# Optimization experiments

Measured on AMD Instinct MI355X. Metric: run time of the kernel, lower is better.

## Reference

```python
import jax, jax.numpy as jnp
import numpy as np

B, S, D, H = 2, 2048, 1024, 16
HD = D // H  # head_dim = 64


def setup_inputs() -> dict:
    key = jax.random.key(0)
    ks = jax.random.split(key, 11)
    init = 1.0 / np.sqrt(D)
    inp = {
        "query": jax.random.normal(ks[0], (B, S, D), jnp.float32),
        "key": jax.random.normal(ks[1], (B, S, D), jnp.float32),
        "value": jax.random.normal(ks[2], (B, S, D), jnp.float32),
        "Wq": jax.random.uniform(ks[3], (D, D), jnp.float32, -init, init),
        "bq": jax.random.uniform(ks[4], (D,), jnp.float32, -init, init),
        "Wk": jax.random.uniform(ks[5], (D, D), jnp.float32, -init, init),
        "bk": jax.random.uniform(ks[6], (D,), jnp.float32, -init, init),
        "Wv": jax.random.uniform(ks[7], (D, D), jnp.float32, -init, init),
        "bv": jax.random.uniform(ks[8], (D,), jnp.float32, -init, init),
        "Wo": jax.random.uniform(ks[9], (D, D), jnp.float32, -init, init),
        "bo": jax.random.uniform(ks[10], (D,), jnp.float32, -init, init),
    }
    return inp


def reference(query, key, value, Wq, bq, Wk, bk, Wv, bv, Wo, bo):
    # Linear projections (torch Linear: x @ W.T + b)
    q = query @ Wq.T + bq  # [B,S,D]
    k = key @ Wk.T + bk
    v = value @ Wv.T + bv
    # split heads -> [B,H,S,HD]
    q = q.reshape(B, S, H, HD).transpose(0, 2, 1, 3)
    k = k.reshape(B, S, H, HD).transpose(0, 2, 1, 3)
    v = v.reshape(B, S, H, HD).transpose(0, 2, 1, 3)
    # NOTE: original code divides by scale = head_dim**-0.5, i.e. multiplies
    # scores by sqrt(head_dim). Reproduced faithfully.
    scale = HD ** (-0.5)
    scores = jnp.einsum("bhqd,bhkd->bhqk", q, k) / scale  # [B,H,S,S]
    attn = jax.nn.softmax(scores, axis=-1)
    x = jnp.einsum("bhqk,bhkd->bhqd", attn, v)  # [B,H,S,HD]
    x = x.transpose(0, 2, 1, 3).reshape(B, S, D)
    return x @ Wo.T + bo
```

## Files before the change

kernel.cpp:

```cpp
#include <hip/hip_runtime.h>
#include <stdint.h>
#include <stddef.h>

#define SCALE_LOG2E 11.541560327111707f
#define E8 4194304
#define M1 1048576
#define NROW 65536

typedef __attribute__((ext_vector_type(8))) _Float16 f16x8;
typedef __attribute__((ext_vector_type(4))) _Float16 f16x4;
typedef __attribute__((ext_vector_type(4))) float f32x4;

#if __has_builtin(__builtin_amdgcn_exp2f)
#define EXP2F(x) __builtin_amdgcn_exp2f(x)
#else
#define EXP2F(x) exp2f(x)
#endif

__device__ __forceinline__ f32x4 mfma_f16(f16x8 a, f16x8 b, f32x4 c) {
  return __builtin_amdgcn_mfma_f32_16x16x32_f16(a, b, c, 0, 0, 0);
}

__device__ __forceinline__ f32x4 mfma16_f16(f16x4 a, f16x4 b, f32x4 c) {
  return __builtin_amdgcn_mfma_f32_16x16x16f16(a, b, c, 0, 0, 0);
}

__device__ __forceinline__ void async16(const void* g, void* lds) {
  __builtin_amdgcn_global_load_lds(
      (const __attribute__((address_space(1))) unsigned int*)g,
      (__attribute__((address_space(3))) unsigned int*)lds, 16, 0, 0);
}

__global__ void prep_all(const float* __restrict__ q, const float* __restrict__ k,
                         const float* __restrict__ v,
                         const float* __restrict__ wq, const float* __restrict__ wk,
                         const float* __restrict__ wv, const float* __restrict__ wo,
                         _Float16* __restrict__ Xf, _Float16* __restrict__ Wf) {
  const int gid = blockIdx.x;
  const float* src;
  _Float16* dst;
  int i;
  if (gid < 6144) {
    const int z = gid >> 11;
    src = (z == 0) ? q : (z == 1) ? k : v;
    dst = Xf + (size_t)z * E8;
    i = (gid & 2047) * 512 + threadIdx.x;
  } else {
    const int g2 = gid - 6144;
    const int z = g2 >> 9;
    src = (z == 0) ? wq : (z == 1) ? wk : (z == 2) ? wv : wo;
    dst = Wf + (size_t)z * M1;
    i = (g2 & 511) * 512 + threadIdx.x;
  }
#pragma unroll
  for (int off = 0; off < 512; off += 256) {
    float4 x = ((const float4*)src)[i + off];
    f16x4 h = {(_Float16)x.x, (_Float16)x.y, (_Float16)x.z, (_Float16)x.w};
    ((f16x4*)dst)[i + off] = h;
  }
}

__global__ __launch_bounds__(256, 3) void gemm_qkv(
    const _Float16* __restrict__ Xf,
    const _Float16* __restrict__ Wf,
    const float* __restrict__ bq, const float* __restrict__ bk,
    const float* __restrict__ bv,
    _Float16* __restrict__ Of)
{
  __shared__ _Float16 SMEM[16384];
  _Float16* LA = SMEM;
  _Float16* LB = SMEM + 8192;
  const int z = blockIdx.z;
  const int tid = threadIdx.x;
  const int lane = tid & 63;
  const int wv = tid >> 6;
  const int wm = wv >> 1, wn = wv & 1;
  const int rl = lane & 15, qd = lane >> 4;
  const int m0 = blockIdx.x * 128, n0 = blockIdx.y * 128;

  const _Float16* A0 = Xf + (size_t)z * E8;
  const _Float16* W0 = Wf + (size_t)z * M1;
  const float* bias = (z == 0) ? bq : (z == 1) ? bk : bv;

  f32x4 acc[4][4];
#pragma unroll
  for (int i = 0; i < 4; i++)
#pragma unroll
    for (int j = 0; j < 4; j++) acc[i][j] = f32x4{0.f, 0.f, 0.f, 0.f};

  const int srow = wv * 32 + (lane >> 2);
  const int scol = (lane & 3) * 8;

  auto stage = [&](int k0, int buf) {
    const _Float16* ga = A0 + (size_t)(m0 + srow) * 1024 + k0 + scol;
    async16(ga, &LA[buf * 4096 + wv * 1024]);
    async16(ga + 16 * 1024, &LA[buf * 4096 + wv * 1024 + 512]);
    const _Float16* gb = W0 + (size_t)(n0 + srow) * 1024 + k0 + scol;
    async16(gb, &LB[buf * 4096 + wv * 1024]);
    async16(gb + 16 * 1024, &LB[buf * 4096 + wv * 1024 + 512]);
  };

  stage(0, 0);
  for (int t = 0; t < 32; t++) {
    const int buf = t & 1;
    __syncthreads();
    if (t + 1 < 32) stage((t + 1) * 32, buf ^ 1);
    f16x8 af[4], bfr[4];
#pragma unroll
    for (int i = 0; i < 4; i++) af[i] = *(const f16x8*)&LA[buf * 4096 + (wm * 64 + i * 16 + rl) * 32 + qd * 8];
#pragma unroll
    for (int j = 0; j < 4; j++) bfr[j] = *(const f16x8*)&LB[buf * 4096 + (wn * 64 + j * 16 + rl) * 32 + qd * 8];
#pragma unroll
    for (int i = 0; i < 4; i++)
#pragma unroll
      for (int j = 0; j < 4; j++) acc[i][j] = mfma_f16(af[i], bfr[j], acc[i][j]);
  }

  if (z == 2) {
#pragma unroll
    for (int j = 0; j < 4; j++) {
      const int nn = n0 + wn * 64 + j * 16 + rl;
      const float bj = bias[nn];
      const int hh = nn >> 6, e = nn & 63;
#pragma unroll
      for (int i = 0; i < 4; i++) {
        const int mm = m0 + wm * 64 + i * 16 + qd * 4;
        const int b = mm >> 11, s = mm & 2047;
        f16x4 pk = {(_Float16)(acc[i][j][0] + bj), (_Float16)(acc[i][j][1] + bj),
                    (_Float16)(acc[i][j][2] + bj), (_Float16)(acc[i][j][3] + bj)};
        *(f16x4*)(Of + 2 * (size_t)E8 + (((size_t)((b * 16 + hh) * 64 + e)) << 11) + s) = pk;
      }
    }
  } else {
    const float scl = (z == 0) ? SCALE_LOG2E : 1.0f;
    _Float16* base = Of + (size_t)z * E8;
    __syncthreads();
#pragma unroll
    for (int j = 0; j < 4; j++) {
      const int nl = wn * 64 + j * 16 + rl;
      const float bj = bias[n0 + nl];
#pragma unroll
      for (int i = 0; i < 4; i++) {
        const int ml = wm * 64 + i * 16 + qd * 4;
        const int np = nl ^ (qd << 4);
#pragma unroll
        for (int r = 0; r < 4; r++)
          SMEM[(ml + r) * 128 + np] = (_Float16)((acc[i][j][r] + bj) * scl);
      }
    }
    __syncthreads();
#pragma unroll
    for (int it2 = 0; it2 < 8; it2++) {
      const int m = (it2 * 256 + tid) >> 4;
      const int col8 = (tid & 15) * 8;
      const int np = col8 ^ (((m >> 2) & 3) << 4);
      f16x8 vrow = *(const f16x8*)&SMEM[m * 128 + np];
      const int sg = m0 + m;
      const int b = sg >> 11, s = sg & 2047;
      const int nn = n0 + col8;
      const int hh = nn >> 6, e = nn & 63;
      *(f16x8*)(base + (((size_t)((b * 16 + hh) * 2048 + s)) << 6) + e) = vrow;
    }
  }
}

__global__ __launch_bounds__(256, 4) void attn_kernel(
    const _Float16* __restrict__ Qb,
    const _Float16* __restrict__ Kb,
    const _Float16* __restrict__ Vt,
    float* __restrict__ Op,
    float2* __restrict__ ML)
{
  __shared__ _Float16 Ks[2][4096];
  __shared__ _Float16 Vs[2][4096];
  const int tid = threadIdx.x;
  const int lane = tid & 63;
  const int wv = tid >> 6;
  const int rl = lane & 15, qd = lane >> 4;
  const int bh = blockIdx.x;
  const int half = blockIdx.z;
  const int kvb = half * 1024;
  const int q0 = blockIdx.y * 128 + wv * 32;

  f16x8 qf[2][2];
#pragma unroll
  for (int mt = 0; mt < 2; mt++)
#pragma unroll
    for (int kk = 0; kk < 2; kk++)
      qf[mt][kk] = *(const f16x8*)(Qb + ((size_t)bh * 2048 + q0 + mt * 16 + rl) * 64 +
                                   kk * 32 + qd * 8);

  float m_[2] = {-1e30f, -1e30f}, l_[2] = {0.f, 0.f};
  f32x4 o[2][4];
#pragma unroll
  for (int mt = 0; mt < 2; mt++)
#pragma unroll
    for (int jt = 0; jt < 4; jt++) o[mt][jt] = f32x4{0.f, 0.f, 0.f, 0.f};

  auto stage = [&](int kv, int buf) {
#pragma unroll
    for (int it = 0; it < 2; it++) {
      const int cI = it * 256 + tid;
      const int row = cI >> 3;
      const int c = (cI & 7) ^ (row & 7);
      const int dst = (it * 256 + wv * 64) * 8;
      async16(Kb + ((size_t)bh * 2048 + kv + row) * 64 + c * 8, &Ks[buf][dst]);
      async16(Vt + ((size_t)bh * 64 + row) * 2048 + kv + c * 8, &Vs[buf][dst]);
    }
  };

  stage(kvb, 0);

  for (int t = 0; t < 16; t++) {
    const int buf = t & 1;
    __syncthreads();
    if (t + 1 < 16) stage(kvb + (t + 1) * 64, buf ^ 1);

    f32x4 sc[2][4];
#pragma unroll
    for (int mt = 0; mt < 2; mt++)
#pragma unroll
      for (int nt = 0; nt < 4; nt++) sc[mt][nt] = f32x4{0.f, 0.f, 0.f, 0.f};
    __builtin_amdgcn_s_setprio(1);
#pragma unroll
    for (int nt = 0; nt < 4; nt++) {
      const int ro = (nt * 16 + rl) * 64;
#pragma unroll
      for (int kk = 0; kk < 2; kk++) {
        const int cc = (((kk * 4 + qd) ^ (rl & 7)) << 3);
        f16x8 kh = *(const f16x8*)&Ks[buf][ro + cc];
#pragma unroll
        for (int mt = 0; mt < 2; mt++)
          sc[mt][nt] = mfma_f16(kh, qf[mt][kk], sc[mt][nt]);
      }
    }
    __builtin_amdgcn_s_setprio(0);

    f16x4 pf[2][4];
#pragma unroll
    for (int mt = 0; mt < 2; mt++) {
      float a0 = fmaxf(fmaxf(sc[mt][0][0], sc[mt][0][1]), fmaxf(sc[mt][0][2], sc[mt][0][3]));
      float a1 = fmaxf(fmaxf(sc[mt][1][0], sc[mt][1][1]), fmaxf(sc[mt][1][2], sc[mt][1][3]));
      float a2 = fmaxf(fmaxf(sc[mt][2][0], sc[mt][2][1]), fmaxf(sc[mt][2][2], sc[mt][2][3]));
      float a3 = fmaxf(fmaxf(sc[mt][3][0], sc[mt][3][1]), fmaxf(sc[mt][3][2], sc[mt][3][3]));
      float mloc = fmaxf(fmaxf(a0, a1), fmaxf(a2, a3));
      float mx = fmaxf(mloc, __shfl_xor(mloc, 16));
      mx = fmaxf(mx, __shfl_xor(mx, 32));
      const float mold = m_[mt];
      float mnew = mold;
      if (__any(mx > mold + 8.f)) {
        mnew = fmaxf(mold, mx);
        const float al = EXP2F(mold - mnew);
        l_[mt] *= al;
#pragma unroll
        for (int jt = 0; jt < 4; jt++)
#pragma unroll
          for (int r = 0; r < 4; r++) o[mt][jt][r] *= al;
        m_[mt] = mnew;
      }
      float sm = 0.f;
#pragma unroll
      for (int nt = 0; nt < 4; nt++) {
        const float p0 = EXP2F(sc[mt][nt][0] - mnew);
        const float p1 = EXP2F(sc[mt][nt][1] - mnew);
        const float p2 = EXP2F(sc[mt][nt][2] - mnew);
        const float p3 = EXP2F(sc[mt][nt][3] - mnew);
        sm += (p0 + p1) + (p2 + p3);
        pf[mt][nt] = f16x4{(_Float16)p0, (_Float16)p1, (_Float16)p2, (_Float16)p3};
      }
      l_[mt] += sm;
    }

    __builtin_amdgcn_s_setprio(1);
#pragma unroll
    for (int nt = 0; nt < 4; nt++) {
      const int cb = nt * 2 + (qd >> 1);
#pragma unroll
      for (int jt = 0; jt < 4; jt++) {
        const int row = jt * 16 + rl;
        f16x4 vvv = *(const f16x4*)&Vs[buf][row * 64 + ((cb ^ (rl & 7)) << 3) + (qd & 1) * 4];
        o[0][jt] = mfma16_f16(vvv, pf[0][nt], o[0][jt]);
        o[1][jt] = mfma16_f16(vvv, pf[1][nt], o[1][jt]);
      }
    }
    __builtin_amdgcn_s_setprio(0);
  }

#pragma unroll
  for (int mt = 0; mt < 2; mt++) {
    float lt = l_[mt] + __shfl_xor(l_[mt], 16);
    lt += __shfl_xor(lt, 32);
    const size_t row = (size_t)bh * 2048 + q0 + mt * 16 + rl;
    float* op = Op + ((size_t)half * NROW + row) * 64;
#pragma unroll
    for (int jt = 0; jt < 4; jt++)
      *(f32x4*)(op + jt * 16 + qd * 4) = o[mt][jt];
    if (qd == 0) ML[(size_t)half * NROW + row] = make_float2(m_[mt], lt);
  }
}

__global__ void merge_kernel(const float* __restrict__ Op,
                             const float2* __restrict__ ML,
                             _Float16* __restrict__ Xo) {
  const int t = threadIdx.x;
  const int row = blockIdx.x * 16 + (t >> 4);
  const int d0 = (t & 15) * 4;
  const float2 ml1 = ML[row];
  const float2 ml2 = ML[NROW + row];
  const float m = fmaxf(ml1.x, ml2.x);
  const float w1 = EXP2F(ml1.x - m), w2 = EXP2F(ml2.x - m);
  const float inv = 1.0f / (ml1.y * w1 + ml2.y * w2);
  const float4 o1 = *(const float4*)(Op + (size_t)row * 64 + d0);
  const float4 o2 = *(const float4*)(Op + (size_t)NROW * 64 + (size_t)row * 64 + d0);
  const int bh = row >> 11, q = row & 2047;
  const int b = bh >> 4, hh = bh & 15;
  f16x4 pk = {(_Float16)((o1.x * w1 + o2.x * w2) * inv),
              (_Float16)((o1.y * w1 + o2.y * w2) * inv),
              (_Float16)((o1.z * w1 + o2.z * w2) * inv),
              (_Float16)((o1.w * w1 + o2.w * w2) * inv)};
  *(f16x4*)(Xo + ((size_t)(b * 2048 + q)) * 1024 + hh * 64 + d0) = pk;
}

__global__ __launch_bounds__(256, 2) void gemm_out(
    const _Float16* __restrict__ A0,
    const _Float16* __restrict__ W0,
    const float* __restrict__ bias,
    float* __restrict__ out)
{
  __shared__ _Float16 LA[2][2048];
  __shared__ _Float16 LB[2][4096];
  const int tid = threadIdx.x;
  const int lane = tid & 63;
  const int wv = tid >> 6;
  const int wm = wv >> 1, wn = wv & 1;
  const int rl = lane & 15, qd = lane >> 4;
  const int m0 = blockIdx.x * 64, n0 = blockIdx.y * 128;

  f32x4 acc[2][4];
#pragma unroll
  for (int i = 0; i < 2; i++)
#pragma unroll
    for (int j = 0; j < 4; j++) acc[i][j] = f32x4{0.f, 0.f, 0.f, 0.f};

  auto stage = [&](int k0, int buf) {
    {
      const int row = tid >> 2, c = tid & 3;
      async16(A0 + (size_t)(m0 + row) * 1024 + k0 + c * 8, &LA[buf][wv * 512]);
    }
#pragma unroll
    for (int it = 0; it < 2; it++) {
      const int cI = it * 256 + tid;
      const int row = cI >> 2, c = cI & 3;
      async16(W0 + (size_t)(n0 + row) * 1024 + k0 + c * 8,
              &LB[buf][it * 2048 + wv * 512]);
    }
  };

  stage(0, 0);
  for (int t = 0; t < 32; t++) {
    const int buf = t & 1;
    __syncthreads();
    if (t + 1 < 32) stage((t + 1) * 32, buf ^ 1);
    f16x8 af[2], bfr[4];
#pragma unroll
    for (int i = 0; i < 2; i++) af[i] = *(const f16x8*)&LA[buf][(wm * 32 + i * 16 + rl) * 32 + qd * 8];
#pragma unroll
    for (int j = 0; j < 4; j++) bfr[j] = *(const f16x8*)&LB[buf][(wn * 64 + j * 16 + rl) * 32 + qd * 8];
#pragma unroll
    for (int i = 0; i < 2; i++)
#pragma unroll
      for (int j = 0; j < 4; j++) acc[i][j] = mfma_f16(af[i], bfr[j], acc[i][j]);
  }

#pragma unroll
  for (int j = 0; j < 4; j++) {
    const int nn = n0 + wn * 64 + j * 16 + rl;
    const float bj = bias[nn];
#pragma unroll
    for (int i = 0; i < 2; i++) {
      const int mm = m0 + wm * 32 + i * 16 + qd * 4;
#pragma unroll
      for (int r = 0; r < 4; r++)
        out[(size_t)(mm + r) * 1024 + nn] = acc[i][j][r] + bj;
    }
  }
}

extern "C" void kernel_launch(void* const* d_in, const int* in_sizes, int n_in,
                              void* d_out, int out_size, void* d_ws, size_t ws_size,
                              hipStream_t stream) {
  const float* query = (const float*)d_in[0];
  const float* key   = (const float*)d_in[1];
  const float* value = (const float*)d_in[2];
  const float* Wq = (const float*)d_in[3];
  const float* bq = (const float*)d_in[4];
  const float* Wk = (const float*)d_in[5];
  const float* bk = (const float*)d_in[6];
  const float* Wv = (const float*)d_in[7];
  const float* bv = (const float*)d_in[8];
  const float* Wo = (const float*)d_in[9];
  const float* bo = (const float*)d_in[10];

  _Float16* ws = (_Float16*)d_ws;
  _Float16* Xf = ws;
  _Float16* Wf = ws + 3 * (size_t)E8;
  _Float16* Qh = Wf + 4 * (size_t)M1;
  _Float16* Kh = Qh + (size_t)E8;
  _Float16* Vt = Kh + (size_t)E8;
  _Float16* Xa = Vt + (size_t)E8;
  float*    Op = (float*)(Xa + (size_t)E8);
  float2*   ML = (float2*)(Op + 2 * (size_t)NROW * 64);

  prep_all<<<8192, 256, 0, stream>>>(query, key, value, Wq, Wk, Wv, Wo, Xf, Wf);
  gemm_qkv<<<dim3(32, 8, 3), 256, 0, stream>>>(Xf, Wf, bq, bk, bv, Qh);
  attn_kernel<<<dim3(32, 16, 2), 256, 0, stream>>>(Qh, Kh, Vt, Op, ML);
  merge_kernel<<<4096, 256, 0, stream>>>(Op, ML, Xa);
  gemm_out<<<dim3(64, 8), 256, 0, stream>>>(Xa, Wf + 3 * (size_t)M1, bo, (float*)d_out);
}
```

Measured before the change: 240.9 us.

## Fuse fp32-to-fp16 activation conversion into QKV GEMM A-tile loading

```diff
diff --git a/kernel.cpp b/kernel.cpp
--- a/kernel.cpp
+++ b/kernel.cpp
@@ -31,29 +31,21 @@
       (__attribute__((address_space(3))) unsigned int*)lds, 16, 0, 0);
 }
 
-__global__ void prep_all(const float* __restrict__ q, const float* __restrict__ k,
-                         const float* __restrict__ v,
-                         const float* __restrict__ wq, const float* __restrict__ wk,
-                         const float* __restrict__ wv, const float* __restrict__ wo,
-                         _Float16* __restrict__ Xf, _Float16* __restrict__ Wf) {
+__device__ __forceinline__ f16x8 cvt8(float4 a, float4 b) {
+  return f16x8{(_Float16)a.x, (_Float16)a.y, (_Float16)a.z, (_Float16)a.w,
+               (_Float16)b.x, (_Float16)b.y, (_Float16)b.z, (_Float16)b.w};
+}
+
+__global__ void prep_w(const float* __restrict__ wq, const float* __restrict__ wk,
+                       const float* __restrict__ wv, const float* __restrict__ wo,
+                       _Float16* __restrict__ Wf) {
   const int gid = blockIdx.x;
-  const float* src;
-  _Float16* dst;
-  int i;
-  if (gid < 6144) {
-    const int z = gid >> 11;
-    src = (z == 0) ? q : (z == 1) ? k : v;
-    dst = Xf + (size_t)z * E8;
-    i = (gid & 2047) * 512 + threadIdx.x;
-  } else {
-    const int g2 = gid - 6144;
-    const int z = g2 >> 9;
-    src = (z == 0) ? wq : (z == 1) ? wk : (z == 2) ? wv : wo;
-    dst = Wf + (size_t)z * M1;
-    i = (g2 & 511) * 512 + threadIdx.x;
-  }
-#pragma unroll
-  for (int off = 0; off < 512; off += 256) {
+  const int z = gid >> 8;
+  const float* src = (z == 0) ? wq : (z == 1) ? wk : (z == 2) ? wv : wo;
+  _Float16* dst = Wf + (size_t)z * M1;
+  const int i = (gid & 255) * 1024 + threadIdx.x;
+#pragma unroll
+  for (int off = 0; off < 1024; off += 256) {
     float4 x = ((const float4*)src)[i + off];
     f16x4 h = {(_Float16)x.x, (_Float16)x.y, (_Float16)x.z, (_Float16)x.w};
     ((f16x4*)dst)[i + off] = h;
@@ -61,7 +53,8 @@
 }
 
 __global__ __launch_bounds__(256, 3) void gemm_qkv(
-    const _Float16* __restrict__ Xf,
+    const float* __restrict__ q32, const float* __restrict__ k32,
+    const float* __restrict__ v32,
     const _Float16* __restrict__ Wf,
     const float* __restrict__ bq, const float* __restrict__ bk,
     const float* __restrict__ bv,
@@ -78,7 +71,7 @@
   const int rl = lane & 15, qd = lane >> 4;
   const int m0 = blockIdx.x * 128, n0 = blockIdx.y * 128;
 
-  const _Float16* A0 = Xf + (size_t)z * E8;
+  const float* A32 = (z == 0) ? q32 : (z == 1) ? k32 : v32;
   const _Float16* W0 = Wf + (size_t)z * M1;
   const float* bias = (z == 0) ? bq : (z == 1) ? bk : bv;
 
@@ -91,20 +84,34 @@
   const int srow = wv * 32 + (lane >> 2);
   const int scol = (lane & 3) * 8;
 
-  auto stage = [&](int k0, int buf) {
-    const _Float16* ga = A0 + (size_t)(m0 + srow) * 1024 + k0 + scol;
-    async16(ga, &LA[buf * 4096 + wv * 1024]);
-    async16(ga + 16 * 1024, &LA[buf * 4096 + wv * 1024 + 512]);
+  auto stageB = [&](int k0, int buf) {
     const _Float16* gb = W0 + (size_t)(n0 + srow) * 1024 + k0 + scol;
     async16(gb, &LB[buf * 4096 + wv * 1024]);
     async16(gb + 16 * 1024, &LB[buf * 4096 + wv * 1024 + 512]);
   };
-
-  stage(0, 0);
+  auto loadA = [&](int k0, float4* ar) {
+    const float* ga = A32 + (size_t)(m0 + srow) * 1024 + k0 + scol;
+    ar[0] = *(const float4*)(ga);
+    ar[1] = *(const float4*)(ga + 4);
+    ar[2] = *(const float4*)(ga + 16 * 1024);
+    ar[3] = *(const float4*)(ga + 16 * 1024 + 4);
+  };
+  auto writeA = [&](int buf, const float4* ar) {
+    *(f16x8*)&LA[buf * 4096 + wv * 1024 + lane * 8] = cvt8(ar[0], ar[1]);
+    *(f16x8*)&LA[buf * 4096 + wv * 1024 + 512 + lane * 8] = cvt8(ar[2], ar[3]);
+  };
+
+  float4 ar[4];
+  loadA(0, ar);
+  stageB(0, 0);
+  writeA(0, ar);
   for (int t = 0; t < 32; t++) {
     const int buf = t & 1;
     __syncthreads();
-    if (t + 1 < 32) stage((t + 1) * 32, buf ^ 1);
+    if (t + 1 < 32) {
+      loadA((t + 1) * 32, ar);
+      stageB((t + 1) * 32, buf ^ 1);
+    }
     f16x8 af[4], bfr[4];
 #pragma unroll
     for (int i = 0; i < 4; i++) af[i] = *(const f16x8*)&LA[buf * 4096 + (wm * 64 + i * 16 + rl) * 32 + qd * 8];
@@ -114,6 +121,7 @@
     for (int i = 0; i < 4; i++)
 #pragma unroll
       for (int j = 0; j < 4; j++) acc[i][j] = mfma_f16(af[i], bfr[j], acc[i][j]);
+    if (t + 1 < 32) writeA(buf ^ 1, ar);
   }
 
   if (z == 2) {
@@ -402,7 +410,6 @@
   const float* bo = (const float*)d_in[10];
 
   _Float16* ws = (_Float16*)d_ws;
-  _Float16* Xf = ws;
   _Float16* Wf = ws + 3 * (size_t)E8;
   _Float16* Qh = Wf + 4 * (size_t)M1;
   _Float16* Kh = Qh + (size_t)E8;
@@ -411,8 +418,8 @@
   float*    Op = (float*)(Xa + (size_t)E8);
   float2*   ML = (float2*)(Op + 2 * (size_t)NROW * 64);
 
-  prep_all<<<8192, 256, 0, stream>>>(query, key, value, Wq, Wk, Wv, Wo, Xf, Wf);
-  gemm_qkv<<<dim3(32, 8, 3), 256, 0, stream>>>(Xf, Wf, bq, bk, bv, Qh);
+  prep_w<<<1024, 256, 0, stream>>>(Wq, Wk, Wv, Wo, Wf);
+  gemm_qkv<<<dim3(32, 8, 3), 256, 0, stream>>>(query, key, value, Wf, bq, bk, bv, Qh);
   attn_kernel<<<dim3(32, 16, 2), 256, 0, stream>>>(Qh, Kh, Vt, Op, ML);
   merge_kernel<<<4096, 256, 0, stream>>>(Op, ML, Xa);
   gemm_out<<<dim3(64, 8), 256, 0, stream>>>(Xa, Wf + 3 * (size_t)M1, bo, (float*)d_out);
```

Measured after the change: 248.6 us. +3.2%, slower.

## Fuse split-KV merge into output projection GEMM A-tile loading

Applied to the files above, without the earlier changes.

```diff
diff --git a/kernel.cpp b/kernel.cpp
--- a/kernel.cpp
+++ b/kernel.cpp
@@ -299,30 +299,9 @@
   }
 }
 
-__global__ void merge_kernel(const float* __restrict__ Op,
-                             const float2* __restrict__ ML,
-                             _Float16* __restrict__ Xo) {
-  const int t = threadIdx.x;
-  const int row = blockIdx.x * 16 + (t >> 4);
-  const int d0 = (t & 15) * 4;
-  const float2 ml1 = ML[row];
-  const float2 ml2 = ML[NROW + row];
-  const float m = fmaxf(ml1.x, ml2.x);
-  const float w1 = EXP2F(ml1.x - m), w2 = EXP2F(ml2.x - m);
-  const float inv = 1.0f / (ml1.y * w1 + ml2.y * w2);
-  const float4 o1 = *(const float4*)(Op + (size_t)row * 64 + d0);
-  const float4 o2 = *(const float4*)(Op + (size_t)NROW * 64 + (size_t)row * 64 + d0);
-  const int bh = row >> 11, q = row & 2047;
-  const int b = bh >> 4, hh = bh & 15;
-  f16x4 pk = {(_Float16)((o1.x * w1 + o2.x * w2) * inv),
-              (_Float16)((o1.y * w1 + o2.y * w2) * inv),
-              (_Float16)((o1.z * w1 + o2.z * w2) * inv),
-              (_Float16)((o1.w * w1 + o2.w * w2) * inv)};
-  *(f16x4*)(Xo + ((size_t)(b * 2048 + q)) * 1024 + hh * 64 + d0) = pk;
-}
-
 __global__ __launch_bounds__(256, 2) void gemm_out(
-    const _Float16* __restrict__ A0,
+    const float* __restrict__ Op,
+    const float2* __restrict__ ML,
     const _Float16* __restrict__ W0,
     const float* __restrict__ bias,
     float* __restrict__ out)
@@ -342,11 +321,11 @@
 #pragma unroll
     for (int j = 0; j < 4; j++) acc[i][j] = f32x4{0.f, 0.f, 0.f, 0.f};
 
-  auto stage = [&](int k0, int buf) {
-    {
-      const int row = tid >> 2, c = tid & 3;
-      async16(A0 + (size_t)(m0 + row) * 1024 + k0 + c * 8, &LA[buf][wv * 512]);
-    }
+  const int arow = tid >> 2, ac = tid & 3;
+  const int am = m0 + arow;
+  const size_t prow_b = (size_t)((am >> 11) * 16) * 2048 + (am & 2047);
+
+  auto stageB = [&](int k0, int buf) {
 #pragma unroll
     for (int it = 0; it < 2; it++) {
       const int cI = it * 256 + tid;
@@ -355,12 +334,44 @@
               &LB[buf][it * 2048 + wv * 512]);
     }
   };
-
-  stage(0, 0);
+  auto loadA = [&](int k0, f32x4* a4, float2& ml1, float2& ml2) {
+    const int hh = k0 >> 6;
+    const size_t prow = prow_b + (size_t)hh * 2048;
+    const int d0 = (k0 & 63) + ac * 8;
+    const float* p1 = Op + prow * 64 + d0;
+    const float* p2 = Op + (size_t)NROW * 64 + prow * 64 + d0;
+    a4[0] = *(const f32x4*)p1;
+    a4[1] = *(const f32x4*)(p1 + 4);
+    a4[2] = *(const f32x4*)p2;
+    a4[3] = *(const f32x4*)(p2 + 4);
+    ml1 = ML[prow];
+    ml2 = ML[NROW + prow];
+  };
+  auto writeA = [&](int buf, const f32x4* a4, float2 ml1, float2 ml2) {
+    const float mm = fmaxf(ml1.x, ml2.x);
+    const float w1 = EXP2F(ml1.x - mm), w2 = EXP2F(ml2.x - mm);
+    const float inv = 1.0f / (ml1.y * w1 + ml2.y * w2);
+    f16x8 hv;
+#pragma unroll
+    for (int j = 0; j < 4; j++) {
+      hv[j]     = (_Float16)((a4[0][j] * w1 + a4[2][j] * w2) * inv);
+      hv[j + 4] = (_Float16)((a4[1][j] * w1 + a4[3][j] * w2) * inv);
+    }
+    *(f16x8*)&LA[buf][tid * 8] = hv;
+  };
+
+  f32x4 a4[4];
+  float2 ml1, ml2;
+  loadA(0, a4, ml1, ml2);
+  stageB(0, 0);
+  writeA(0, a4, ml1, ml2);
   for (int t = 0; t < 32; t++) {
     const int buf = t & 1;
     __syncthreads();
-    if (t + 1 < 32) stage((t + 1) * 32, buf ^ 1);
+    if (t + 1 < 32) {
+      loadA((t + 1) * 32, a4, ml1, ml2);
+      stageB((t + 1) * 32, buf ^ 1);
+    }
     f16x8 af[2], bfr[4];
 #pragma unroll
     for (int i = 0; i < 2; i++) af[i] = *(const f16x8*)&LA[buf][(wm * 32 + i * 16 + rl) * 32 + qd * 8];
@@ -370,6 +381,7 @@
     for (int i = 0; i < 2; i++)
 #pragma unroll
       for (int j = 0; j < 4; j++) acc[i][j] = mfma_f16(af[i], bfr[j], acc[i][j]);
+    if (t + 1 < 32) writeA(buf ^ 1, a4, ml1, ml2);
   }
 
 #pragma unroll
@@ -414,6 +426,5 @@
   prep_all<<<8192, 256, 0, stream>>>(query, key, value, Wq, Wk, Wv, Wo, Xf, Wf);
   gemm_qkv<<<dim3(32, 8, 3), 256, 0, stream>>>(Xf, Wf, bq, bk, bv, Qh);
   attn_kernel<<<dim3(32, 16, 2), 256, 0, stream>>>(Qh, Kh, Vt, Op, ML);
-  merge_kernel<<<4096, 256, 0, stream>>>(Op, ML, Xa);
-  gemm_out<<<dim3(64, 8), 256, 0, stream>>>(Xa, Wf + 3 * (size_t)M1, bo, (float*)d_out);
-}
+  gemm_out<<<dim3(64, 8), 256, 0, stream>>>(Op, ML, Wf + 3 * (size_t)M1, bo, (float*)d_out);
+}
```

New measurement: 249.5 us. +3.5%, slower.

## Drop split-KV attention and merge kernel; process full KV per block

Applied to the files above, without the earlier changes.

```diff
diff --git a/kernel.cpp b/kernel.cpp
--- a/kernel.cpp
+++ b/kernel.cpp
@@ -5,7 +5,6 @@
 #define SCALE_LOG2E 11.541560327111707f
 #define E8 4194304
 #define M1 1048576
-#define NROW 65536
 
 typedef __attribute__((ext_vector_type(8))) _Float16 f16x8;
 typedef __attribute__((ext_vector_type(4))) _Float16 f16x4;
@@ -168,8 +167,7 @@
     const _Float16* __restrict__ Qb,
     const _Float16* __restrict__ Kb,
     const _Float16* __restrict__ Vt,
-    float* __restrict__ Op,
-    float2* __restrict__ ML)
+    _Float16* __restrict__ Xo)
 {
   __shared__ _Float16 Ks[2][4096];
   __shared__ _Float16 Vs[2][4096];
@@ -178,24 +176,17 @@
   const int wv = tid >> 6;
   const int rl = lane & 15, qd = lane >> 4;
   const int bh = blockIdx.x;
-  const int half = blockIdx.z;
-  const int kvb = half * 1024;
-  const int q0 = blockIdx.y * 128 + wv * 32;
-
-  f16x8 qf[2][2];
-#pragma unroll
-  for (int mt = 0; mt < 2; mt++)
-#pragma unroll
-    for (int kk = 0; kk < 2; kk++)
-      qf[mt][kk] = *(const f16x8*)(Qb + ((size_t)bh * 2048 + q0 + mt * 16 + rl) * 64 +
-                                   kk * 32 + qd * 8);
-
-  float m_[2] = {-1e30f, -1e30f}, l_[2] = {0.f, 0.f};
-  f32x4 o[2][4];
-#pragma unroll
-  for (int mt = 0; mt < 2; mt++)
-#pragma unroll
-    for (int jt = 0; jt < 4; jt++) o[mt][jt] = f32x4{0.f, 0.f, 0.f, 0.f};
+  const int q0 = blockIdx.y * 64 + wv * 16;
+
+  f16x8 qf[2];
+#pragma unroll
+  for (int kk = 0; kk < 2; kk++)
+    qf[kk] = *(const f16x8*)(Qb + ((size_t)bh * 2048 + q0 + rl) * 64 + kk * 32 + qd * 8);
+
+  float m_ = -1e30f, l_ = 0.f;
+  f32x4 o[4];
+#pragma unroll
+  for (int jt = 0; jt < 4; jt++) o[jt] = f32x4{0.f, 0.f, 0.f, 0.f};
 
   auto stage = [&](int kv, int buf) {
 #pragma unroll
@@ -209,18 +200,16 @@
     }
   };
 
-  stage(kvb, 0);
-
-  for (int t = 0; t < 16; t++) {
+  stage(0, 0);
+
+  for (int t = 0; t < 32; t++) {
     const int buf = t & 1;
     __syncthreads();
-    if (t + 1 < 16) stage(kvb + (t + 1) * 64, buf ^ 1);
-
-    f32x4 sc[2][4];
-#pragma unroll
-    for (int mt = 0; mt < 2; mt++)
-#pragma unroll
-      for (int nt = 0; nt < 4; nt++) sc[mt][nt] = f32x4{0.f, 0.f, 0.f, 0.f};
+    if (t + 1 < 32) stage((t + 1) * 64, buf ^ 1);
+
+    f32x4 sc[4];
+#pragma unroll
+    for (int nt = 0; nt < 4; nt++) sc[nt] = f32x4{0.f, 0.f, 0.f, 0.f};
     __builtin_amdgcn_s_setprio(1);
 #pragma unroll
     for (int nt = 0; nt < 4; nt++) {
@@ -229,46 +218,43 @@
       for (int kk = 0; kk < 2; kk++) {
         const int cc = (((kk * 4 + qd) ^ (rl & 7)) << 3);
         f16x8 kh = *(const f16x8*)&Ks[buf][ro + cc];
-#pragma unroll
-        for (int mt = 0; mt < 2; mt++)
-          sc[mt][nt] = mfma_f16(kh, qf[mt][kk], sc[mt][nt]);
+        sc[nt] = mfma_f16(kh, qf[kk], sc[nt]);
       }
     }
     __builtin_amdgcn_s_setprio(0);
 
-    f16x4 pf[2][4];
-#pragma unroll
-    for (int mt = 0; mt < 2; mt++) {
-      float a0 = fmaxf(fmaxf(sc[mt][0][0], sc[mt][0][1]), fmaxf(sc[mt][0][2], sc[mt][0][3]));
-      float a1 = fmaxf(fmaxf(sc[mt][1][0], sc[mt][1][1]), fmaxf(sc[mt][1][2], sc[mt][1][3]));
-      float a2 = fmaxf(fmaxf(sc[mt][2][0], sc[mt][2][1]), fmaxf(sc[mt][2][2], sc[mt][2][3]));
-      float a3 = fmaxf(fmaxf(sc[mt][3][0], sc[mt][3][1]), fmaxf(sc[mt][3][2], sc[mt][3][3]));
+    f16x4 pf[4];
+    {
+      float a0 = fmaxf(fmaxf(sc[0][0], sc[0][1]), fmaxf(sc[0][2], sc[0][3]));
+      float a1 = fmaxf(fmaxf(sc[1][0], sc[1][1]), fmaxf(sc[1][2], sc[1][3]));
+      float a2 = fmaxf(fmaxf(sc[2][0], sc[2][1]), fmaxf(sc[2][2], sc[2][3]));
+      float a3 = fmaxf(fmaxf(sc[3][0], sc[3][1]), fmaxf(sc[3][2], sc[3][3]));
       float mloc = fmaxf(fmaxf(a0, a1), fmaxf(a2, a3));
       float mx = fmaxf(mloc, __shfl_xor(mloc, 16));
       mx = fmaxf(mx, __shfl_xor(mx, 32));
-      const float mold = m_[mt];
+      const float mold = m_;
       float mnew = mold;
       if (__any(mx > mold + 8.f)) {
         mnew = fmaxf(mold, mx);
         const float al = EXP2F(mold - mnew);
-        l_[mt] *= al;
+        l_ *= al;
 #pragma unroll
         for (int jt = 0; jt < 4; jt++)
 #pragma unroll
-          for (int r = 0; r < 4; r++) o[mt][jt][r] *= al;
-        m_[mt] = mnew;
+          for (int r = 0; r < 4; r++) o[jt][r] *= al;
+        m_ = mnew;
       }
       float sm = 0.f;
 #pragma unroll
       for (int nt = 0; nt < 4; nt++) {
-        const float p0 = EXP2F(sc[mt][nt][0] - mnew);
-        const float p1 = EXP2F(sc[mt][nt][1] - mnew);
-        const float p2 = EXP2F(sc[mt][nt][2] - mnew);
-        const float p3 = EXP2F(sc[mt][nt][3] - mnew);
+        const float p0 = EXP2F(sc[nt][0] - mnew);
+        const float p1 = EXP2F(sc[nt][1] - mnew);
+        const float p2 = EXP2F(sc[nt][2] - mnew);
+        const float p3 = EXP2F(sc[nt][3] - mnew);
         sm += (p0 + p1) + (p2 + p3);
-        pf[mt][nt] = f16x4{(_Float16)p0, (_Float16)p1, (_Float16)p2, (_Float16)p3};
-      }
-      l_[mt] += sm;
+        pf[nt] = f16x4{(_Float16)p0, (_Float16)p1, (_Float16)p2, (_Float16)p3};
+      }
+      l_ += sm;
     }
 
     __builtin_amdgcn_s_setprio(1);
@@ -279,46 +265,26 @@
       for (int jt = 0; jt < 4; jt++) {
         const int row = jt * 16 + rl;
         f16x4 vvv = *(const f16x4*)&Vs[buf][row * 64 + ((cb ^ (rl & 7)) << 3) + (qd & 1) * 4];
-        o[0][jt] = mfma16_f16(vvv, pf[0][nt], o[0][jt]);
-        o[1][jt] = mfma16_f16(vvv, pf[1][nt], o[1][jt]);
+        o[jt] = mfma16_f16(vvv, pf[nt], o[jt]);
       }
     }
     __builtin_amdgcn_s_setprio(0);
   }
 
-#pragma unroll
-  for (int mt = 0; mt < 2; mt++) {
-    float lt = l_[mt] + __shfl_xor(l_[mt], 16);
+  {
+    float lt = l_ + __shfl_xor(l_, 16);
     lt += __shfl_xor(lt, 32);
-    const size_t row = (size_t)bh * 2048 + q0 + mt * 16 + rl;
-    float* op = Op + ((size_t)half * NROW + row) * 64;
-#pragma unroll
-    for (int jt = 0; jt < 4; jt++)
-      *(f32x4*)(op + jt * 16 + qd * 4) = o[mt][jt];
-    if (qd == 0) ML[(size_t)half * NROW + row] = make_float2(m_[mt], lt);
-  }
-}
-
-__global__ void merge_kernel(const float* __restrict__ Op,
-                             const float2* __restrict__ ML,
-                             _Float16* __restrict__ Xo) {
-  const int t = threadIdx.x;
-  const int row = blockIdx.x * 16 + (t >> 4);
-  const int d0 = (t & 15) * 4;
-  const float2 ml1 = ML[row];
-  const float2 ml2 = ML[NROW + row];
-  const float m = fmaxf(ml1.x, ml2.x);
-  const float w1 = EXP2F(ml1.x - m), w2 = EXP2F(ml2.x - m);
-  const float inv = 1.0f / (ml1.y * w1 + ml2.y * w2);
-  const float4 o1 = *(const float4*)(Op + (size_t)row * 64 + d0);
-  const float4 o2 = *(const float4*)(Op + (size_t)NROW * 64 + (size_t)row * 64 + d0);
-  const int bh = row >> 11, q = row & 2047;
-  const int b = bh >> 4, hh = bh & 15;
-  f16x4 pk = {(_Float16)((o1.x * w1 + o2.x * w2) * inv),
-              (_Float16)((o1.y * w1 + o2.y * w2) * inv),
-              (_Float16)((o1.z * w1 + o2.z * w2) * inv),
-              (_Float16)((o1.w * w1 + o2.w * w2) * inv)};
-  *(f16x4*)(Xo + ((size_t)(b * 2048 + q)) * 1024 + hh * 64 + d0) = pk;
+    const float inv = 1.0f / lt;
+    const int b = bh >> 4, hh = bh & 15;
+    const int s = q0 + rl;
+    _Float16* xp = Xo + ((size_t)(b * 2048 + s)) * 1024 + hh * 64;
+#pragma unroll
+    for (int jt = 0; jt < 4; jt++) {
+      f16x4 pk = {(_Float16)(o[jt][0] * inv), (_Float16)(o[jt][1] * inv),
+                  (_Float16)(o[jt][2] * inv), (_Float16)(o[jt][3] * inv)};
+      *(f16x4*)(xp + jt * 16 + qd * 4) = pk;
+    }
+  }
 }
 
 __global__ __launch_bounds__(256, 2) void gemm_out(
@@ -408,12 +374,9 @@
   _Float16* Kh = Qh + (size_t)E8;
   _Float16* Vt = Kh + (size_t)E8;
   _Float16* Xa = Vt + (size_t)E8;
-  float*    Op = (float*)(Xa + (size_t)E8);
-  float2*   ML = (float2*)(Op + 2 * (size_t)NROW * 64);
 
   prep_all<<<8192, 256, 0, stream>>>(query, key, value, Wq, Wk, Wv, Wo, Xf, Wf);
   gemm_qkv<<<dim3(32, 8, 3), 256, 0, stream>>>(Xf, Wf, bq, bk, bv, Qh);
-  attn_kernel<<<dim3(32, 16, 2), 256, 0, stream>>>(Qh, Kh, Vt, Op, ML);
-  merge_kernel<<<4096, 256, 0, stream>>>(Op, ML, Xa);
+  attn_kernel<<<dim3(32, 32), 256, 0, stream>>>(Qh, Kh, Vt, Xa);
   gemm_out<<<dim3(64, 8), 256, 0, stream>>>(Xa, Wf + 3 * (size_t)M1, bo, (float*)d_out);
 }
```

Result: faster. 232.3 us (-3.6%).
